# Kernel optimization log

Hardware: AMD Instinct MI355X
Metric: run time of the kernel (lower is better)

Reference implementation:

```python
import jax, jax.numpy as jnp
import numpy as np

TEMPERATURE = 0.1
NORMALIZED = True


def _l2norm(x, eps=1e-12):
    # matches F.normalize(p=2, dim=1)
    n = jnp.sqrt(jnp.sum(x * x, axis=1, keepdims=True))
    return x / jnp.maximum(n, eps)


def setup_inputs() -> dict:
    key = jax.random.key(0)
    k1, k2, k3, k4 = jax.random.split(key, 4)
    B, D = 4096, 256
    return {
        "hs": jax.random.normal(k1, (B, D), dtype=jnp.float32),
        "ht0": jax.random.normal(k2, (B, D), dtype=jnp.float32),
        "ht1": jax.random.normal(k3, (B, D), dtype=jnp.float32),
        "labels": jax.random.randint(k4, (B,), 0, 100, dtype=jnp.int64)
        if jax.config.jax_enable_x64 else jax.random.randint(k4, (B,), 0, 100, dtype=jnp.int32),
        "num_views": 2,
    }


def _per_teacher_loss(hs_n, ht_n, mask, logits_mask, batch_size, num_views):
    # features: [N, D] with N = 2B
    features = jnp.concatenate([hs_n, ht_n], axis=0)
    sim = jnp.matmul(features, features.T) / TEMPERATURE          # [N, N]
    exp_logits = jnp.exp(sim) * logits_mask                        # [N, N]
    log_prob = sim - jnp.log(jnp.sum(exp_logits, axis=1, keepdims=True))
    per_inst = -jnp.sum(mask * log_prob, axis=1) / jnp.sum(mask, axis=1)  # [N]
    if num_views > 1:
        per_inst = per_inst.reshape(batch_size, num_views).mean(axis=1)
    return per_inst.mean()


def reference(hs, ht0, ht1, labels, num_views):
    batch_size = labels.shape[0]
    hs = hs.reshape(batch_size, -1)
    ht_list = [ht0.reshape(batch_size, -1), ht1.reshape(batch_size, -1)]
    if NORMALIZED:
        hs = _l2norm(hs)
        ht_list = [_l2norm(ht) for ht in ht_list]

    labels2 = jnp.concatenate([labels, labels])                    # [N]
    mask = (labels2[:, None] == labels2[None, :]).astype(jnp.float32)
    N = 2 * batch_size
    logits_mask = 1.0 - jnp.eye(N, dtype=jnp.float32)              # zero diagonal
    mask = mask * logits_mask

    inter_loss = 0.0
    for ht in ht_list:
        inter_loss = inter_loss + _per_teacher_loss(
            hs, ht, mask, logits_mask, batch_size, num_views)
    return inter_loss / len(ht_list)
```

## Files before the change

kernel.cpp:

```cpp
#include <hip/hip_runtime.h>
#include <hip/hip_bf16.h>

#define B_SIZE 4096
#define D_SIZE 256
#define N_SIZE 8192
#define LOG2E10 14.4269504089f

typedef __attribute__((ext_vector_type(8))) short short8;
typedef __attribute__((ext_vector_type(4))) short short4v;
typedef __attribute__((ext_vector_type(4))) float floatx4;


__device__ __forceinline__ void async16(void* lds, const void* g) {
    __builtin_amdgcn_global_load_lds(
        (const __attribute__((address_space(1))) unsigned int*)g,
        (__attribute__((address_space(3))) unsigned int*)lds, 16, 0, 0);
}

__global__ void norm_kernel(const float* __restrict__ hs,
                            const float* __restrict__ ht0,
                            const float* __restrict__ ht1,
                            __hip_bfloat16* __restrict__ dst,
                            float* __restrict__ zero_region,
                            const int* __restrict__ labels,
                            int* __restrict__ cnt, int* __restrict__ offv,
                            int* __restrict__ idxS) {
    int id  = blockIdx.x;
    int tid = threadIdx.x;
    int gid = id * 256 + tid;
    if (gid < 16386) zero_region[gid] = 0.0f;

    const float* src = (id < 4096) ? (hs + id * D_SIZE)
                     : (id < 8192) ? (ht0 + (id - 4096) * D_SIZE)
                                   : (ht1 + (id - 8192) * D_SIZE);
    float x = src[tid];
    float ss = x * x;
#pragma unroll
    for (int off = 32; off > 0; off >>= 1) ss += __shfl_xor(ss, off);
    __shared__ float wsum[4];
    int wave = tid >> 6, lane = tid & 63;
    if (lane == 0) wsum[wave] = ss;
    __syncthreads();
    float tot = wsum[0] + wsum[1] + wsum[2] + wsum[3];
    float inv = 1.0f / fmaxf(sqrtf(tot), 1e-12f);
    dst[id * D_SIZE + tid] = __float2bfloat16(x * inv);

    if (id == 0) {
        __shared__ int h[128], o[128], ctr[128];
        if (tid < 128) { h[tid] = 0; ctr[tid] = 0; }
        __syncthreads();
        for (int i = tid; i < B_SIZE; i += 256) atomicAdd(&h[labels[i] & 127], 1);
        __syncthreads();
        if (tid == 0) {
            int s = 0;
            for (int c = 0; c < 128; ++c) { o[c] = s; s += h[c]; }
        }
        __syncthreads();
        for (int i = tid; i < B_SIZE; i += 256) {
            int lab = labels[i] & 127;
            int pos = o[lab] + atomicAdd(&ctr[lab], 1);
            idxS[pos] = i;
        }
        if (tid < 128) { cnt[tid] = h[tid]; offv[tid] = o[tid]; }
    }
}

__global__ void gvec_kernel(const __hip_bfloat16* __restrict__ featBase,
                            const int* __restrict__ cnt,
                            const int* __restrict__ off,
                            const int* __restrict__ idxS,
                            float* __restrict__ gOut) {
    const int c   = blockIdx.x & 127;
    const int set = blockIdx.x >> 7;
    const int tid = threadIdx.x;
    const __hip_bfloat16* f = featBase + set * B_SIZE * D_SIZE;
    __shared__ int sIdx[256];
    const int n = cnt[c], o = off[c];
    float acc = 0.0f;
    for (int base = 0; base < n; base += 256) {
        int m = n - base; if (m > 256) m = 256;
        __syncthreads();
        if (tid < m) sIdx[tid] = idxS[o + base + tid];
        __syncthreads();
        for (int k = 0; k < m; ++k)
            acc += __bfloat162float(f[sIdx[k] * D_SIZE + tid]);
    }
    gOut[set * 32768 + c * 256 + tid] = acc;
}

__global__ __launch_bounds__(256, 2)
void sim_kernel(const __hip_bfloat16* __restrict__ featS,
                const __hip_bfloat16* __restrict__ featT0,
                const __hip_bfloat16* __restrict__ featT1,
                float* __restrict__ Sarr) {
    __shared__ __align__(16) unsigned char sB[2][32768];

    const int p = blockIdx.x;
    const int t = blockIdx.y;
    const __hip_bfloat16* featT = t ? featT1 : featT0;

    int R = (int)((sqrtf((float)(8 * p + 1)) - 1.0f) * 0.5f);
    while ((R + 1) * (R + 2) / 2 <= p) ++R;
    while (R * (R + 1) / 2 > p) --R;
    const int C = p - R * (R + 1) / 2;

    const int tid  = threadIdx.x;
    const int w    = tid >> 6;
    const int l    = tid & 63;
    const int quad = l >> 4;
    const int lcol = l & 15;
    const int row_base = R * 256 + w * 64;

    short8 af[4][8];
#pragma unroll
    for (int rt = 0; rt < 4; ++rt) {
        int arow = row_base + rt * 16 + lcol;
        const __hip_bfloat16* ap = (arow < B_SIZE) ? featS + arow * D_SIZE
                                                   : featT + (arow - B_SIZE) * D_SIZE;
#pragma unroll
        for (int ks = 0; ks < 8; ++ks)
            af[rt][ks] = *reinterpret_cast<const short8*>(ap + ks * 32 + quad * 8);
    }

    float Sp[4][4];
#pragma unroll
    for (int rt = 0; rt < 4; ++rt)
#pragma unroll
        for (int r = 0; r < 4; ++r) Sp[rt][r] = 0.0f;

    const int col0 = C * 256;

    auto stage = [&](int b, int cb) {
        int tb = cb + w * 16;
        const __hip_bfloat16* cp = (tb < B_SIZE) ? featS + tb * D_SIZE
                                                 : featT + (tb - B_SIZE) * D_SIZE;
        const char* gp = (const char*)cp + (l & 15) * 512 + (l >> 4) * 16;
        unsigned char* lp = &sB[b][w * 8192];
#pragma unroll
        for (int ks = 0; ks < 8; ++ks)
            async16(lp + ks * 1024, gp + ks * 64);
    };

    stage(0, col0);

    for (int g = 0; g < 4; ++g) {
        const int buf = g & 1;
        __syncthreads();
        if (g + 1 < 4) stage(buf ^ 1, col0 + (g + 1) * 64);

        const int gcol = col0 + g * 64;
        if (gcol > row_base) continue;
        const bool diag = (gcol == row_base);

        float Cp[4] = {0.f, 0.f, 0.f, 0.f};
#pragma unroll
        for (int up = 0; up < 2; ++up) {
            floatx4 acc[2][4];
#pragma unroll
            for (int j = 0; j < 2; ++j)
#pragma unroll
                for (int rt = 0; rt < 4; ++rt) acc[j][rt] = floatx4{0.f, 0.f, 0.f, 0.f};

#pragma unroll
            for (int ks = 0; ks < 8; ++ks) {
                short8 bf[2];
#pragma unroll
                for (int j = 0; j < 2; ++j)
                    bf[j] = *reinterpret_cast<const short8*>(
                        &sB[buf][(up * 2 + j) * 8192 + ks * 1024 + l * 16]);
#pragma unroll
                for (int j = 0; j < 2; ++j)
#pragma unroll
                    for (int rt = 0; rt < 4; ++rt)
                        acc[j][rt] = __builtin_amdgcn_mfma_f32_16x16x32_bf16(
                            af[rt][ks], bf[j], acc[j][rt], 0, 0, 0);
            }
#pragma unroll
            for (int j = 0; j < 2; ++j)
#pragma unroll
                for (int rt = 0; rt < 4; ++rt)
#pragma unroll
                    for (int r = 0; r < 4; ++r) {
                        float e = exp2f(acc[j][rt][r] * LOG2E10);
                        Sp[rt][r] += e;
                        Cp[up * 2 + j] += e;
                    }
        }

        if (!diag) {
#pragma unroll
            for (int u = 0; u < 4; ++u) {
                Cp[u] += __shfl_xor(Cp[u], 16);
                Cp[u] += __shfl_xor(Cp[u], 32);
            }
            if (quad == 0) {
#pragma unroll
                for (int u = 0; u < 4; ++u)
                    atomicAdd(&Sarr[t * N_SIZE + gcol + u * 16 + lcol], Cp[u]);
            }
        }
    }

#pragma unroll
    for (int rt = 0; rt < 4; ++rt)
#pragma unroll
        for (int r = 0; r < 4; ++r) {
#pragma unroll
            for (int m = 1; m < 16; m <<= 1) Sp[rt][r] += __shfl_xor(Sp[rt][r], m);
        }
    if (lcol == 0) {
#pragma unroll
        for (int rt = 0; rt < 4; ++rt)
#pragma unroll
            for (int r = 0; r < 4; ++r) {
                int row = row_base + rt * 16 + quad * 4 + r;
                atomicAdd(&Sarr[t * N_SIZE + row], Sp[rt][r]);
            }
    }
}

__global__ void rowstat_kernel(const __hip_bfloat16* __restrict__ featS,
                               const __hip_bfloat16* __restrict__ featT0,
                               const __hip_bfloat16* __restrict__ featT1,
                               const int* __restrict__ labels,
                               const float* __restrict__ gAll,
                               const int* __restrict__ cnt,
                               const float* __restrict__ Sarr,
                               float* __restrict__ lossAcc,
                               int* __restrict__ ticket,
                               float* __restrict__ out) {
    __shared__ float wpart[4];
    const int tid = threadIdx.x;
    const int wv  = tid >> 6;
    const int l   = tid & 63;
    const int waveid = blockIdx.x * 4 + wv;
    float psum = 0.0f;

    for (int it = 0; it < 8; ++it) {
        int R = waveid * 8 + it;
        int t = R >> 13;
        int i = R & (N_SIZE - 1);
        const __hip_bfloat16* f = (i < B_SIZE) ? featS + i * D_SIZE
                                : (t ? featT1 : featT0) + (i - B_SIZE) * D_SIZE;
        int lab = labels[i & (B_SIZE - 1)] & 127;
        short4v fb = *reinterpret_cast<const short4v*>(f + l * 4);
        float fx[4];
#pragma unroll
        for (int k = 0; k < 4; ++k) {
            unsigned int u = ((unsigned int)(unsigned short)fb[k]) << 16;
            fx[k] = __uint_as_float(u);
        }
        const float* gS = gAll + lab * 256 + l * 4;
        const float* gT = gAll + (1 + t) * 32768 + lab * 256 + l * 4;
        float dot = 0.f, aii = 0.f;
#pragma unroll
        for (int k = 0; k < 4; ++k) {
            dot += fx[k] * (gS[k] + gT[k]);
            aii += fx[k] * fx[k];
        }
#pragma unroll
        for (int m = 1; m < 64; m <<= 1) {
            dot += __shfl_xor(dot, m);
            aii += __shfl_xor(aii, m);
        }
        if (l == 0) {
            float S = Sarr[t * N_SIZE + i];
            float M = 2.0f * (float)cnt[lab] - 1.0f;
            float E = exp2f(LOG2E10 * aii);
            psum += logf(S - E) - 10.0f * (dot - aii) / M;
        }
    }
    if (l == 0) wpart[wv] = psum;
    __syncthreads();
    if (tid == 0) {
        atomicAdd(lossAcc, wpart[0] + wpart[1] + wpart[2] + wpart[3]);
        __threadfence();
        if (atomicAdd(ticket, 1) == 511) {
            float tot = atomicAdd(lossAcc, 0.0f);
            out[0] = tot / 16384.0f;
        }
    }
}

extern "C" void kernel_launch(void* const* d_in, const int* in_sizes, int n_in,
                              void* d_out, int out_size, void* d_ws, size_t ws_size,
                              hipStream_t stream) {
    const float* hs     = (const float*)d_in[0];
    const float* ht0    = (const float*)d_in[1];
    const float* ht1    = (const float*)d_in[2];
    const int*   labels = (const int*)d_in[3];

    char* ws = (char*)d_ws;
    float* Sarr    = (float*)(ws);
    float* lossAcc = (float*)(ws + 65536);
    int*   ticket  = (int*)(ws + 65540);
    int*   cnt     = (int*)(ws + 66048);
    int*   offv    = (int*)(ws + 66560);
    int*   idxS    = (int*)(ws + 67072);
    float* gAll    = (float*)(ws + 83968);
    __hip_bfloat16* featS  = (__hip_bfloat16*)(ws + 524288);
    __hip_bfloat16* featT0 = (__hip_bfloat16*)(ws + 524288 + 2097152);
    __hip_bfloat16* featT1 = (__hip_bfloat16*)(ws + 524288 + 2 * 2097152);

    norm_kernel<<<3 * 4096, 256, 0, stream>>>(hs, ht0, ht1, featS, (float*)ws,
                                              labels, cnt, offv, idxS);
    gvec_kernel<<<384, 256, 0, stream>>>(featS, cnt, offv, idxS, gAll);
    sim_kernel<<<dim3(528, 2), 256, 0, stream>>>(featS, featT0, featT1, Sarr);
    rowstat_kernel<<<512, 256, 0, stream>>>(featS, featT0, featT1, labels, gAll, cnt,
                                            Sarr, lossAcc, ticket, (float*)d_out);
}
```

Before: 165.8 us.

## Balance sim tile work across 512 blocks, vectorize normalization, use fast exp2

The sim kernel replaces its 528x2 triangular grid with 512 blocks. Each block handles two or three tile items: off-diagonal pairs first, and the cheaper diagonal tiles are grouped three to a block, so per-block work is even and the grid fits in one wave of residency. The norm kernel now processes one row per wave using float4 loads with no LDS reduction or barrier, and launches a quarter as many blocks. exp2f is replaced by the hardware exp2 builtin. The changes add per-block serialization of items and slightly lower exp precision.

```diff
diff --git a/kernel.cpp b/kernel.cpp
--- a/kernel.cpp
+++ b/kernel.cpp
@@ -6,6 +6,12 @@
 #define N_SIZE 8192
 #define LOG2E10 14.4269504089f
 
+#if __has_builtin(__builtin_amdgcn_exp2f)
+#define FAST_EXP2(x) __builtin_amdgcn_exp2f(x)
+#else
+#define FAST_EXP2(x) __expf((x) * 0.69314718056f)
+#endif
+
 typedef __attribute__((ext_vector_type(8))) short short8;
 typedef __attribute__((ext_vector_type(4))) short short4v;
 typedef __attribute__((ext_vector_type(4))) float floatx4;
@@ -15,6 +21,13 @@
     __builtin_amdgcn_global_load_lds(
         (const __attribute__((address_space(1))) unsigned int*)g,
         (__attribute__((address_space(3))) unsigned int*)lds, 16, 0, 0);
+}
+
+__device__ __forceinline__ void pair_from_q(int q, int& R, int& C) {
+    int r = (int)((1.0f + sqrtf(1.0f + 8.0f * (float)q)) * 0.5f);
+    while (r * (r - 1) / 2 > q) --r;
+    while ((r + 1) * r / 2 <= q) ++r;
+    R = r; C = q - r * (r - 1) / 2;
 }
 
 __global__ void norm_kernel(const float* __restrict__ hs,
@@ -25,43 +38,46 @@
                             const int* __restrict__ labels,
                             int* __restrict__ cnt, int* __restrict__ offv,
                             int* __restrict__ idxS) {
-    int id  = blockIdx.x;
-    int tid = threadIdx.x;
-    int gid = id * 256 + tid;
+    const int tid = threadIdx.x;
+    const int wv  = tid >> 6;
+    const int l   = tid & 63;
+    const int gid = blockIdx.x * 256 + tid;
     if (gid < 16386) zero_region[gid] = 0.0f;
 
-    const float* src = (id < 4096) ? (hs + id * D_SIZE)
-                     : (id < 8192) ? (ht0 + (id - 4096) * D_SIZE)
-                                   : (ht1 + (id - 8192) * D_SIZE);
-    float x = src[tid];
-    float ss = x * x;
+    const int row = blockIdx.x * 4 + wv;
+    const float* src = (row < 4096) ? (hs + row * D_SIZE)
+                     : (row < 8192) ? (ht0 + (row - 4096) * D_SIZE)
+                                    : (ht1 + (row - 8192) * D_SIZE);
+    floatx4 x = *reinterpret_cast<const floatx4*>(src + l * 4);
+    float ss = x[0] * x[0] + x[1] * x[1] + x[2] * x[2] + x[3] * x[3];
 #pragma unroll
     for (int off = 32; off > 0; off >>= 1) ss += __shfl_xor(ss, off);
-    __shared__ float wsum[4];
-    int wave = tid >> 6, lane = tid & 63;
-    if (lane == 0) wsum[wave] = ss;
-    __syncthreads();
-    float tot = wsum[0] + wsum[1] + wsum[2] + wsum[3];
-    float inv = 1.0f / fmaxf(sqrtf(tot), 1e-12f);
-    dst[id * D_SIZE + tid] = __float2bfloat16(x * inv);
-
-    if (id == 0) {
-        __shared__ int h[128], o[128], ctr[128];
+    float inv = 1.0f / fmaxf(sqrtf(ss), 1e-12f);
+    short4v o;
+#pragma unroll
+    for (int k = 0; k < 4; ++k) {
+        __hip_bfloat16 h = __float2bfloat16(x[k] * inv);
+        o[k] = *reinterpret_cast<short*>(&h);
+    }
+    *reinterpret_cast<short4v*>(dst + row * D_SIZE + l * 4) = o;
+
+    if (blockIdx.x == 0) {
+        __shared__ int h[128], o2[128], ctr[128];
         if (tid < 128) { h[tid] = 0; ctr[tid] = 0; }
         __syncthreads();
         for (int i = tid; i < B_SIZE; i += 256) atomicAdd(&h[labels[i] & 127], 1);
         __syncthreads();
         if (tid == 0) {
             int s = 0;
-            for (int c = 0; c < 128; ++c) { o[c] = s; s += h[c]; }
+            for (int c = 0; c < 128; ++c) { o2[c] = s; s += h[c]; }
         }
         __syncthreads();
         for (int i = tid; i < B_SIZE; i += 256) {
             int lab = labels[i] & 127;
-            int pos = o[lab] + atomicAdd(&ctr[lab], 1);
+            int pos = o2[lab] + atomicAdd(&ctr[lab], 1);
             idxS[pos] = i;
         }
-        if (tid < 128) { cnt[tid] = h[tid]; offv[tid] = o[tid]; }
+        if (tid < 128) { cnt[tid] = h[tid]; offv[tid] = o2[tid]; }
     }
 }
 
@@ -95,127 +111,141 @@
                 float* __restrict__ Sarr) {
     __shared__ __align__(16) unsigned char sB[2][32768];
 
-    const int p = blockIdx.x;
-    const int t = blockIdx.y;
-    const __hip_bfloat16* featT = t ? featT1 : featT0;
-
-    int R = (int)((sqrtf((float)(8 * p + 1)) - 1.0f) * 0.5f);
-    while ((R + 1) * (R + 2) / 2 <= p) ++R;
-    while (R * (R + 1) / 2 > p) --R;
-    const int C = p - R * (R + 1) / 2;
-
     const int tid  = threadIdx.x;
     const int w    = tid >> 6;
     const int l    = tid & 63;
     const int quad = l >> 4;
     const int lcol = l & 15;
-    const int row_base = R * 256 + w * 64;
-
-    short8 af[4][8];
-#pragma unroll
-    for (int rt = 0; rt < 4; ++rt) {
-        int arow = row_base + rt * 16 + lcol;
-        const __hip_bfloat16* ap = (arow < B_SIZE) ? featS + arow * D_SIZE
-                                                   : featT + (arow - B_SIZE) * D_SIZE;
-#pragma unroll
-        for (int ks = 0; ks < 8; ++ks)
-            af[rt][ks] = *reinterpret_cast<const short8*>(ap + ks * 32 + quad * 8);
-    }
-
-    float Sp[4][4];
-#pragma unroll
-    for (int rt = 0; rt < 4; ++rt)
-#pragma unroll
-        for (int r = 0; r < 4; ++r) Sp[rt][r] = 0.0f;
-
-    const int col0 = C * 256;
-
-    auto stage = [&](int b, int cb) {
-        int tb = cb + w * 16;
-        const __hip_bfloat16* cp = (tb < B_SIZE) ? featS + tb * D_SIZE
-                                                 : featT + (tb - B_SIZE) * D_SIZE;
-        const char* gp = (const char*)cp + (l & 15) * 512 + (l >> 4) * 16;
-        unsigned char* lp = &sB[b][w * 8192];
-#pragma unroll
-        for (int ks = 0; ks < 8; ++ks)
-            async16(lp + ks * 1024, gp + ks * 64);
-    };
-
-    stage(0, col0);
-
-    for (int g = 0; g < 4; ++g) {
-        const int buf = g & 1;
-        __syncthreads();
-        if (g + 1 < 4) stage(buf ^ 1, col0 + (g + 1) * 64);
-
-        const int gcol = col0 + g * 64;
-        if (gcol > row_base) continue;
-        const bool diag = (gcol == row_base);
-
-        float Cp[4] = {0.f, 0.f, 0.f, 0.f};
-#pragma unroll
-        for (int up = 0; up < 2; ++up) {
-            floatx4 acc[2][4];
-#pragma unroll
-            for (int j = 0; j < 2; ++j)
-#pragma unroll
-                for (int rt = 0; rt < 4; ++rt) acc[j][rt] = floatx4{0.f, 0.f, 0.f, 0.f};
-
-#pragma unroll
-            for (int ks = 0; ks < 8; ++ks) {
-                short8 bf[2];
+
+    int itemR[3], itemC[3], itemT[3], ni;
+    if (blockIdx.x < 480) {
+        ni = 2;
+#pragma unroll
+        for (int k = 0; k < 2; ++k) {
+            int m = blockIdx.x * 2 + k;
+            pair_from_q(m >> 1, itemR[k], itemC[k]);
+            itemT[k] = m & 1;
+        }
+    } else {
+        ni = 3;
+        int i = blockIdx.x - 480;
+        int m = 960 + i;
+        pair_from_q(m >> 1, itemR[0], itemC[0]);
+        itemT[0] = m & 1;
+        itemR[1] = itemC[1] = i; itemT[1] = 0;
+        itemR[2] = itemC[2] = i; itemT[2] = 1;
+    }
+
+    for (int it = 0; it < ni; ++it) {
+        const int R = itemR[it], C = itemC[it], t = itemT[it];
+        const __hip_bfloat16* featT = t ? featT1 : featT0;
+        const int row_base = R * 256 + w * 64;
+        const int col0 = C * 256;
+
+        short8 af[4][8];
+#pragma unroll
+        for (int rt = 0; rt < 4; ++rt) {
+            int arow = row_base + rt * 16 + lcol;
+            const __hip_bfloat16* ap = (arow < B_SIZE) ? featS + arow * D_SIZE
+                                                       : featT + (arow - B_SIZE) * D_SIZE;
+#pragma unroll
+            for (int ks = 0; ks < 8; ++ks)
+                af[rt][ks] = *reinterpret_cast<const short8*>(ap + ks * 32 + quad * 8);
+        }
+
+        float Sp[4][4];
+#pragma unroll
+        for (int rt = 0; rt < 4; ++rt)
+#pragma unroll
+            for (int r = 0; r < 4; ++r) Sp[rt][r] = 0.0f;
+
+        auto stage = [&](int b, int cb) {
+            int tb = cb + w * 16;
+            const __hip_bfloat16* cp = (tb < B_SIZE) ? featS + tb * D_SIZE
+                                                     : featT + (tb - B_SIZE) * D_SIZE;
+            const char* gp = (const char*)cp + (l & 15) * 512 + (l >> 4) * 16;
+            unsigned char* lp = &sB[b][w * 8192];
+#pragma unroll
+            for (int ks = 0; ks < 8; ++ks)
+                async16(lp + ks * 1024, gp + ks * 64);
+        };
+
+        stage(0, col0);
+
+        for (int g = 0; g < 4; ++g) {
+            const int buf = g & 1;
+            __syncthreads();
+            if (g + 1 < 4) stage(buf ^ 1, col0 + (g + 1) * 64);
+
+            const int gcol = col0 + g * 64;
+            if (gcol > row_base) continue;
+            const bool dg = (gcol == row_base);
+
+            float Cp[4] = {0.f, 0.f, 0.f, 0.f};
+#pragma unroll
+            for (int up = 0; up < 2; ++up) {
+                floatx4 acc[2][4];
 #pragma unroll
                 for (int j = 0; j < 2; ++j)
-                    bf[j] = *reinterpret_cast<const short8*>(
-                        &sB[buf][(up * 2 + j) * 8192 + ks * 1024 + l * 16]);
+#pragma unroll
+                    for (int rt = 0; rt < 4; ++rt) acc[j][rt] = floatx4{0.f, 0.f, 0.f, 0.f};
+
+#pragma unroll
+                for (int ks = 0; ks < 8; ++ks) {
+                    short8 bf[2];
+#pragma unroll
+                    for (int j = 0; j < 2; ++j)
+                        bf[j] = *reinterpret_cast<const short8*>(
+                            &sB[buf][(up * 2 + j) * 8192 + ks * 1024 + l * 16]);
+#pragma unroll
+                    for (int j = 0; j < 2; ++j)
+#pragma unroll
+                        for (int rt = 0; rt < 4; ++rt)
+                            acc[j][rt] = __builtin_amdgcn_mfma_f32_16x16x32_bf16(
+                                af[rt][ks], bf[j], acc[j][rt], 0, 0, 0);
+                }
 #pragma unroll
                 for (int j = 0; j < 2; ++j)
 #pragma unroll
                     for (int rt = 0; rt < 4; ++rt)
-                        acc[j][rt] = __builtin_amdgcn_mfma_f32_16x16x32_bf16(
-                            af[rt][ks], bf[j], acc[j][rt], 0, 0, 0);
+#pragma unroll
+                        for (int r = 0; r < 4; ++r) {
+                            float e = FAST_EXP2(acc[j][rt][r] * LOG2E10);
+                            Sp[rt][r] += e;
+                            Cp[up * 2 + j] += e;
+                        }
             }
-#pragma unroll
-            for (int j = 0; j < 2; ++j)
-#pragma unroll
-                for (int rt = 0; rt < 4; ++rt)
-#pragma unroll
-                    for (int r = 0; r < 4; ++r) {
-                        float e = exp2f(acc[j][rt][r] * LOG2E10);
-                        Sp[rt][r] += e;
-                        Cp[up * 2 + j] += e;
-                    }
-        }
-
-        if (!diag) {
-#pragma unroll
-            for (int u = 0; u < 4; ++u) {
-                Cp[u] += __shfl_xor(Cp[u], 16);
-                Cp[u] += __shfl_xor(Cp[u], 32);
+
+            if (!dg) {
+#pragma unroll
+                for (int u = 0; u < 4; ++u) {
+                    Cp[u] += __shfl_xor(Cp[u], 16);
+                    Cp[u] += __shfl_xor(Cp[u], 32);
+                }
+                if (quad == 0) {
+#pragma unroll
+                    for (int u = 0; u < 4; ++u)
+                        atomicAdd(&Sarr[t * N_SIZE + gcol + u * 16 + lcol], Cp[u]);
+                }
             }
-            if (quad == 0) {
-#pragma unroll
-                for (int u = 0; u < 4; ++u)
-                    atomicAdd(&Sarr[t * N_SIZE + gcol + u * 16 + lcol], Cp[u]);
+        }
+
+#pragma unroll
+        for (int rt = 0; rt < 4; ++rt)
+#pragma unroll
+            for (int r = 0; r < 4; ++r) {
+#pragma unroll
+                for (int m = 1; m < 16; m <<= 1) Sp[rt][r] += __shfl_xor(Sp[rt][r], m);
             }
-        }
-    }
-
-#pragma unroll
-    for (int rt = 0; rt < 4; ++rt)
-#pragma unroll
-        for (int r = 0; r < 4; ++r) {
-#pragma unroll
-            for (int m = 1; m < 16; m <<= 1) Sp[rt][r] += __shfl_xor(Sp[rt][r], m);
-        }
-    if (lcol == 0) {
-#pragma unroll
-        for (int rt = 0; rt < 4; ++rt)
-#pragma unroll
-            for (int r = 0; r < 4; ++r) {
-                int row = row_base + rt * 16 + quad * 4 + r;
-                atomicAdd(&Sarr[t * N_SIZE + row], Sp[rt][r]);
-            }
+        if (lcol == 0) {
+#pragma unroll
+            for (int rt = 0; rt < 4; ++rt)
+#pragma unroll
+                for (int r = 0; r < 4; ++r) {
+                    int row = row_base + rt * 16 + quad * 4 + r;
+                    atomicAdd(&Sarr[t * N_SIZE + row], Sp[rt][r]);
+                }
+        }
     }
 }
 
@@ -266,7 +296,7 @@
         if (l == 0) {
             float S = Sarr[t * N_SIZE + i];
             float M = 2.0f * (float)cnt[lab] - 1.0f;
-            float E = exp2f(LOG2E10 * aii);
+            float E = FAST_EXP2(LOG2E10 * aii);
             psum += logf(S - E) - 10.0f * (dot - aii) / M;
         }
     }
@@ -302,10 +332,10 @@
     __hip_bfloat16* featT0 = (__hip_bfloat16*)(ws + 524288 + 2097152);
     __hip_bfloat16* featT1 = (__hip_bfloat16*)(ws + 524288 + 2 * 2097152);
 
-    norm_kernel<<<3 * 4096, 256, 0, stream>>>(hs, ht0, ht1, featS, (float*)ws,
-                                              labels, cnt, offv, idxS);
+    norm_kernel<<<3072, 256, 0, stream>>>(hs, ht0, ht1, featS, (float*)ws,
+                                          labels, cnt, offv, idxS);
     gvec_kernel<<<384, 256, 0, stream>>>(featS, cnt, offv, idxS, gAll);
-    sim_kernel<<<dim3(528, 2), 256, 0, stream>>>(featS, featT0, featT1, Sarr);
+    sim_kernel<<<512, 256, 0, stream>>>(featS, featT0, featT1, Sarr);
     rowstat_kernel<<<512, 256, 0, stream>>>(featS, featT0, featT1, labels, gAll, cnt,
                                             Sarr, lossAcc, ticket, (float*)d_out);
 }
```

After: 176.2 us. 1.06x slower.
